# Performance work log

Measured on AMD Instinct MI355X. Metric: run time of the kernel, lower is better.

Reference implementation:

```python
import jax, jax.numpy as jnp
import numpy as np

B, S, HID, NH, HD = 2, 2048, 1024, 16, 64
SCALE = 1.0 / np.sqrt(HD)
NEG = -1e9


def _rope_cache(seq_len, dim, base=10000.0):
    inv_freq = 1.0 / (base ** (np.arange(0, dim, 2, dtype=np.float32) / dim))
    t = np.arange(seq_len, dtype=np.float32)
    freqs = np.outer(t, inv_freq)                      # [S, dim/2]
    emb = np.concatenate([freqs, freqs], axis=-1)      # [S, dim]
    return jnp.asarray(np.cos(emb)), jnp.asarray(np.sin(emb))


def _rotate_half(x):
    x1, x2 = jnp.split(x, 2, axis=-1)
    return jnp.concatenate([-x2, x1], axis=-1)


def setup_inputs() -> dict:
    key = jax.random.key(0)
    k0, k1, k2, k3, k4 = jax.random.split(key, 5)
    hidden_states = jax.random.normal(k0, (B, S, HID), jnp.float32)
    Wq = jax.random.normal(k1, (HID, NH * HD), jnp.float32) * 0.02
    Wk = jax.random.normal(k2, (HID, NH * HD), jnp.float32) * 0.02
    Wv = jax.random.normal(k3, (HID, NH * HD), jnp.float32) * 0.02
    Wo = jax.random.normal(k4, (NH * HD, HID), jnp.float32) * 0.02
    causal = jnp.tril(jnp.ones((S, S), bool))
    attention_mask = jnp.broadcast_to(
        jnp.where(causal, 0.0, NEG).astype(jnp.float32)[None, None], (B, 1, S, S))
    position_ids = jnp.broadcast_to(jnp.arange(S, dtype=jnp.int32)[None], (B, S))
    cos, sin = _rope_cache(S, HD)
    return {"hidden_states": hidden_states, "attention_mask": attention_mask,
            "position_ids": position_ids, "cos": cos, "sin": sin,
            "Wq": Wq, "Wk": Wk, "Wv": Wv, "Wo": Wo}


def reference(hidden_states, attention_mask, position_ids, cos, sin, Wq, Wk, Wv, Wo):
    b, s, _ = hidden_states.shape
    def proj(W):  # [B,S,HID] @ [HID,NH*HD] -> [B,NH,S,HD]
        return jnp.einsum('bsh,hd->bsd', hidden_states, W).reshape(b, s, NH, HD).transpose(0, 2, 1, 3)
    q, k, v = proj(Wq), proj(Wk), proj(Wv)
    # RoPE: gather per-position cos/sin -> [B,1,S,HD]
    cos_g = cos[position_ids][:, None]
    sin_g = sin[position_ids][:, None]
    q = q * cos_g + _rotate_half(q) * sin_g
    k = k * cos_g + _rotate_half(k) * sin_g
    scores = jnp.einsum('bhqd,bhkd->bhqk', q, k) * SCALE + attention_mask
    attn = jax.nn.softmax(scores.astype(jnp.float32), axis=-1).astype(q.dtype)
    out = jnp.einsum('bhqk,bhkd->bhqd', attn, v)
    out = out.transpose(0, 2, 1, 3).reshape(b, s, NH * HD)
    return jnp.einsum('bsd,dh->bsh', out, Wo)
```

## Files before the change

kernel.cpp:

```cpp
#include <hip/hip_runtime.h>

typedef __bf16 bf16x8 __attribute__((ext_vector_type(8)));
typedef float  f32x4  __attribute__((ext_vector_type(4)));
typedef unsigned short ushortx8 __attribute__((ext_vector_type(8)));
typedef unsigned short ushortx4 __attribute__((ext_vector_type(4)));

static __device__ __forceinline__ unsigned short f2bf(float f) {
  unsigned int u = __builtin_bit_cast(unsigned int, f);
  u += 0x7FFFu + ((u >> 16) & 1u);
  return (unsigned short)(u >> 16);
}
static __device__ __forceinline__ unsigned short f2bf_fast(float f) {
  unsigned int u = __builtin_bit_cast(unsigned int, f);
  return (unsigned short)((u + 0x8000u) >> 16);
}

#define GLL16(gp, lp) __builtin_amdgcn_global_load_lds(                       \
    (const __attribute__((address_space(1))) void*)(gp),                      \
    (__attribute__((address_space(3))) void*)(lp), 16, 0, 0)

__global__ __launch_bounds__(256) void cast_x_kernel(const float* __restrict__ x,
                                                     unsigned short* __restrict__ o) {
  long i = ((long)blockIdx.x * 256 + threadIdx.x) * 8;
  float4 f0 = *(const float4*)(x + i);
  float4 f1 = *(const float4*)(x + i + 4);
  ushortx8 u;
  u[0] = f2bf(f0.x); u[1] = f2bf(f0.y); u[2] = f2bf(f0.z); u[3] = f2bf(f0.w);
  u[4] = f2bf(f1.x); u[5] = f2bf(f1.y); u[6] = f2bf(f1.z); u[7] = f2bf(f1.w);
  *(ushortx8*)(o + i) = u;
}

__global__ __launch_bounds__(256) void tpose_w_kernel(const float* __restrict__ W0,
                                                      const float* __restrict__ W1,
                                                      const float* __restrict__ W2,
                                                      const float* __restrict__ W3,
                                                      unsigned short* __restrict__ D0,
                                                      unsigned short* __restrict__ D1,
                                                      unsigned short* __restrict__ D2,
                                                      unsigned short* __restrict__ D3) {
  int z = blockIdx.z;
  const float* src = (z == 0) ? W0 : (z == 1) ? W1 : (z == 2) ? W2 : W3;
  unsigned short* dst = (z == 0) ? D0 : (z == 1) ? D1 : (z == 2) ? D2 : D3;
  const int R = 1024, C = 1024;
  __shared__ unsigned short t[32][33];
  int c = blockIdx.x * 32 + threadIdx.x;
#pragma unroll
  for (int i = 0; i < 4; ++i) {
    int r = blockIdx.y * 32 + threadIdx.y + i * 8;
    t[threadIdx.y + i * 8][threadIdx.x] = f2bf(src[(size_t)r * C + c]);
  }
  __syncthreads();
  int rr = blockIdx.y * 32 + threadIdx.x;
#pragma unroll
  for (int i = 0; i < 4; ++i) {
    int cc = blockIdx.x * 32 + threadIdx.y + i * 8;
    dst[(size_t)cc * R + rr] = t[threadIdx.x][threadIdx.y + i * 8];
  }
}

__global__ __launch_bounds__(256) void tpose_kernel(const unsigned short* __restrict__ src,
                                                    unsigned short* __restrict__ dst,
                                                    int R, int C) {
  size_t moff = (size_t)blockIdx.z * (size_t)R * (size_t)C;
  src += moff; dst += moff;
  __shared__ unsigned short t[32][33];
  int c = blockIdx.x * 32 + threadIdx.x;
#pragma unroll
  for (int i = 0; i < 4; ++i) {
    int r = blockIdx.y * 32 + threadIdx.y + i * 8;
    t[threadIdx.y + i * 8][threadIdx.x] = src[(size_t)r * C + c];
  }
  __syncthreads();
  int rr = blockIdx.y * 32 + threadIdx.x;
#pragma unroll
  for (int i = 0; i < 4; ++i) {
    int cc = blockIdx.x * 32 + threadIdx.y + i * 8;
    dst[(size_t)cc * R + rr] = t[threadIdx.x][threadIdx.y + i * 8];
  }
}

template <int MODE>
__global__ __launch_bounds__(256) void gemm128_kernel(
    const unsigned short* __restrict__ A,
    const unsigned short* __restrict__ BT0,
    const unsigned short* __restrict__ BT1,
    const unsigned short* __restrict__ BT2,
    float* __restrict__ outF,
    unsigned short* __restrict__ outQ,
    unsigned short* __restrict__ outK,
    unsigned short* __restrict__ outV,
    const int* __restrict__ pos_ids,
    const float* __restrict__ cosb,
    const float* __restrict__ sinb) {
  const int K = 1024, N = 1024;
  int z = blockIdx.z;
  const unsigned short* BT = (MODE == 0 || z == 0) ? BT0 : (z == 1 ? BT1 : BT2);
  int n0 = blockIdx.x * 128, m0 = blockIdx.y * 128;
  int t = threadIdx.x, lane = t & 63, w = t >> 6;
  int wy = w >> 1, wx = w & 1;
  int n16 = lane & 15, quad = lane >> 4;
  __shared__ __align__(16) unsigned short sA[128 * 64];
  __shared__ __align__(16) unsigned short sB[128 * 64];

  int r8 = lane >> 3, c8 = lane & 7;
  int srow = w * 32 + r8;
  const char* gA = (const char*)(A + (size_t)(m0 + srow) * K) + (c8 ^ r8) * 16;
  const char* gB = (const char*)(BT + (size_t)(n0 + srow) * K) + (c8 ^ r8) * 16;

  f32x4 acc[4][4];
#pragma unroll
  for (int i = 0; i < 4; ++i)
#pragma unroll
    for (int j = 0; j < 4; ++j) acc[i][j] = f32x4{0.f, 0.f, 0.f, 0.f};

  for (int kk = 0; kk < K; kk += 64) {
    __syncthreads();
#pragma unroll
    for (int i = 0; i < 4; ++i) {
      GLL16(gA + (size_t)kk * 2 + (size_t)i * 8 * K * 2, sA + (w * 32 + i * 8) * 64);
      GLL16(gB + (size_t)kk * 2 + (size_t)i * 8 * K * 2, sB + (w * 32 + i * 8) * 64);
    }
    __syncthreads();
#pragma unroll
    for (int kb = 0; kb < 2; ++kb) {
      bf16x8 a[4], b[4];
#pragma unroll
      for (int i = 0; i < 4; ++i) {
        int ra = wy * 64 + i * 16 + n16;
        int rb = wx * 64 + i * 16 + n16;
        int cs = ((kb * 4 + quad) ^ (n16 & 7)) * 8;
        a[i] = *(const bf16x8*)(&sA[ra * 64 + cs]);
        b[i] = *(const bf16x8*)(&sB[rb * 64 + cs]);
      }
#pragma unroll
      for (int mt = 0; mt < 4; ++mt)
#pragma unroll
        for (int nt = 0; nt < 4; ++nt)
          acc[mt][nt] = __builtin_amdgcn_mfma_f32_16x16x32_bf16(a[mt], b[nt], acc[mt][nt], 0, 0, 0);
    }
  }

  if (MODE == 1 && z < 2) {
#pragma unroll
    for (int mt = 0; mt < 4; ++mt)
#pragma unroll
      for (int r = 0; r < 4; ++r) {
        int row = m0 + wy * 64 + mt * 16 + quad * 4 + r;
        int b = row >> 11, s = row & 2047;
        int pos = pos_ids[b * 2048 + s];
        const float* cb = cosb + (size_t)pos * 64;
        const float* sb = sinb + (size_t)pos * 64;
#pragma unroll
        for (int nt = 0; nt < 2; ++nt) {
          int d0 = nt * 16 + n16;
          float c0 = cb[d0], s0 = sb[d0], c1 = cb[d0 + 32], s1 = sb[d0 + 32];
          float x0 = acc[mt][nt][r], x1 = acc[mt][nt + 2][r];
          acc[mt][nt][r]     = x0 * c0 - x1 * s0;
          acc[mt][nt + 2][r] = x1 * c1 + x0 * s1;
        }
      }
  }

#pragma unroll
  for (int mt = 0; mt < 4; ++mt)
#pragma unroll
    for (int nt = 0; nt < 4; ++nt)
#pragma unroll
      for (int r = 0; r < 4; ++r) {
        int row = m0 + wy * 64 + mt * 16 + quad * 4 + r;
        int col = n0 + wx * 64 + nt * 16 + n16;
        float v = acc[mt][nt][r];
        if (MODE == 0) {
          outF[(size_t)row * N + col] = v;
        } else {
          unsigned short* dst = (z == 0) ? outQ : (z == 1 ? outK : outV);
          int b = row >> 11, s = row & 2047, h = col >> 6, d = col & 63;
          dst[(((size_t)b * 16 + h) * 2048 + s) * 64 + d] = f2bf(v);
        }
      }
}

__global__ __launch_bounds__(256) void attn_kernel(const unsigned short* __restrict__ Q,
                                                   const unsigned short* __restrict__ Kk,
                                                   const unsigned short* __restrict__ VT,
                                                   unsigned short* __restrict__ O) {
  int bh = blockIdx.x;
  int qt = (int)(gridDim.y - 1 - blockIdx.y);
  int t = threadIdx.x;
  int lane = t & 63;
  int w = t >> 6;
  int n16 = lane & 15, quad = lane >> 4;
  int r8 = lane >> 3, c8 = lane & 7;
  const unsigned short* Qb = Q + (size_t)bh * 2048 * 64;
  const unsigned short* Kb = Kk + (size_t)bh * 2048 * 64;
  const unsigned short* Vb = VT + (size_t)bh * 64 * 2048;

  __shared__ __align__(16) unsigned short sK0[64 * 64];
  __shared__ __align__(16) unsigned short sK1[64 * 64];
  __shared__ __align__(16) unsigned short sV0[64 * 64];
  __shared__ __align__(16) unsigned short sV1[64 * 64];
  __shared__ __align__(16) unsigned short sP[4][16 * 64];
  unsigned short* spW = sP[w];

  const float SCL2 = 0.125f * 1.44269504088896340736f;
  int b_ = bh >> 4, h_ = bh & 15;
  int nk = qt + 1;
  int qg = qt * 64 + w * 16 + n16;

  bf16x8 aQ[2];
#pragma unroll
  for (int kb = 0; kb < 2; ++kb)
    aQ[kb] = *(const bf16x8*)(Qb + (size_t)qg * 64 + kb * 32 + quad * 8);

  f32x4 o[4];
  float mst = -3e38f, lst = 0.f;
#pragma unroll
  for (int ct = 0; ct < 4; ++ct) o[ct] = f32x4{0.f, 0.f, 0.f, 0.f};

#define STAGE(kt_, SKB, SVB)                                                              \
  do {                                                                                    \
    const unsigned short* kg_ = Kb + (size_t)((kt_) * 64 + w * 16) * 64;                  \
    const unsigned short* vg_ = Vb + (size_t)(w * 16) * 2048 + (kt_) * 64;                \
    GLL16(kg_ + (size_t)r8 * 64 + (c8 ^ r8) * 8, &SKB[(w * 16) * 64]);                    \
    GLL16(kg_ + (size_t)(8 + r8) * 64 + (c8 ^ r8) * 8, &SKB[(w * 16 + 8) * 64]);          \
    GLL16(vg_ + (size_t)r8 * 2048 + (c8 ^ r8) * 8, &SVB[(w * 16) * 64]);                  \
    GLL16(vg_ + (size_t)(8 + r8) * 2048 + (c8 ^ r8) * 8, &SVB[(w * 16 + 8) * 64]);        \
  } while (0)

#define COMPUTE(kt_, SKB, SVB)                                                            \
  do {                                                                                    \
    f32x4 sc[4];                          \
    _Pragma("unroll") for (int mt = 0; mt < 4; ++mt) {                                    \
      const unsigned short* kr = &SKB[(mt * 16 + n16) * 64];                              \
      bf16x8 ka0 = *(const bf16x8*)(kr + ((quad ^ (n16 & 7)) * 8));                       \
      bf16x8 ka1 = *(const bf16x8*)(kr + (((4 + quad) ^ (n16 & 7)) * 8));                 \
      f32x4 zv = f32x4{0.f, 0.f, 0.f, 0.f};                                               \
      zv = __builtin_amdgcn_mfma_f32_16x16x32_bf16(ka0, aQ[0], zv, 0, 0, 0);              \
      sc[mt] = __builtin_amdgcn_mfma_f32_16x16x32_bf16(ka1, aQ[1], zv, 0, 0, 0);          \
    }                                                                                     \
    float p[4][4];                                                                        \
    _Pragma("unroll") for (int mt = 0; mt < 4; ++mt)                                      \
      _Pragma("unroll") for (int r = 0; r < 4; ++r) p[mt][r] = sc[mt][r] * SCL2;          \
    if ((kt_) == nk - 1) {                                 \
      int kb0 = (kt_) * 64 + quad * 4;                                                    \
      _Pragma("unroll") for (int mt = 0; mt < 4; ++mt)                                    \
        _Pragma("unroll") for (int r = 0; r < 4; ++r)                                     \
          if (kb0 + mt * 16 + r > qg) p[mt][r] = -3e38f;                                  \
    }                                                                                     \
    float rm = p[0][0];                                                                   \
    _Pragma("unroll") for (int mt = 0; mt < 4; ++mt)                                      \
      _Pragma("unroll") for (int r = 0; r < 4; ++r) rm = fmaxf(rm, p[mt][r]);             \
    rm = fmaxf(rm, __shfl_xor(rm, 16));                                                   \
    rm = fmaxf(rm, __shfl_xor(rm, 32));                                                   \
    float mn = fmaxf(mst, rm);                                                            \
    float al = exp2f(mst - mn);                                                           \
    mst = mn;                                                                             \
    float rs = 0.f;                                                                       \
    _Pragma("unroll") for (int mt = 0; mt < 4; ++mt)                                      \
      _Pragma("unroll") for (int r = 0; r < 4; ++r) {                                     \
        p[mt][r] = exp2f(p[mt][r] - mn);                                                  \
        rs += p[mt][r];                                                                   \
      }                                                                                   \
    lst = lst * al + rs;        \
    _Pragma("unroll") for (int ct = 0; ct < 4; ++ct)                                      \
      _Pragma("unroll") for (int r = 0; r < 4; ++r) o[ct][r] *= al;                       \
                   \
    _Pragma("unroll") for (int mt = 0; mt < 4; ++mt) {                                    \
      ushortx4 u;                                                                         \
      _Pragma("unroll") for (int r = 0; r < 4; ++r) u[r] = f2bf_fast(p[mt][r]);           \
      int ch = (mt * 2 + (quad >> 1)) ^ (n16 & 7);                                        \
      *(ushortx4*)(&spW[n16 * 64 + ch * 8 + (quad & 1) * 4]) = u;                         \
    }                                                                                     \
    __builtin_amdgcn_s_waitcnt(0xC07F);   \
    bf16x8 aP0 = *(const bf16x8*)(&spW[n16 * 64 + ((quad ^ (n16 & 7)) * 8)]);             \
    bf16x8 aP1 = *(const bf16x8*)(&spW[n16 * 64 + (((4 + quad) ^ (n16 & 7)) * 8)]);       \
    _Pragma("unroll") for (int ct = 0; ct < 4; ++ct) {                                    \
      const unsigned short* vr = &SVB[(ct * 16 + n16) * 64];                              \
      bf16x8 va0 = *(const bf16x8*)(vr + ((quad ^ (n16 & 7)) * 8));                       \
      bf16x8 va1 = *(const bf16x8*)(vr + (((4 + quad) ^ (n16 & 7)) * 8));                 \
      o[ct] = __builtin_amdgcn_mfma_f32_16x16x32_bf16(va0, aP0, o[ct], 0, 0, 0);          \
      o[ct] = __builtin_amdgcn_mfma_f32_16x16x32_bf16(va1, aP1, o[ct], 0, 0, 0);          \
    }                                                                                     \
  } while (0)

  STAGE(0, sK0, sV0);
  int kt = 0;
  while (true) {
    __syncthreads();
    if (kt + 1 < nk) STAGE(kt + 1, sK1, sV1);
    COMPUTE(kt, sK0, sV0);
    if (++kt == nk) break;
    __syncthreads();
    if (kt + 1 < nk) STAGE(kt + 1, sK0, sV0);
    COMPUTE(kt, sK1, sV1);
    if (++kt == nk) break;
  }
#undef STAGE
#undef COMPUTE

  lst += __shfl_xor(lst, 16);
  lst += __shfl_xor(lst, 32);
  float inv = 1.0f / lst;

#pragma unroll
  for (int ct = 0; ct < 4; ++ct) {
    ushortx4 u;
#pragma unroll
    for (int r = 0; r < 4; ++r) u[r] = f2bf(o[ct][r] * inv);
    size_t addr = ((size_t)b_ * 2048 + qg) * 1024 + h_ * 64 + ct * 16 + quad * 4;
    *(ushortx4*)(&O[addr]) = u;
  }
}

extern "C" void kernel_launch(void* const* d_in, const int* in_sizes, int n_in,
                              void* d_out, int out_size, void* d_ws, size_t ws_size,
                              hipStream_t stream) {
  const float* X    = (const float*)d_in[0];
  const int*   pos  = (const int*)d_in[2];
  const float* cosb = (const float*)d_in[3];
  const float* sinb = (const float*)d_in[4];
  const float* Wq   = (const float*)d_in[5];
  const float* Wk   = (const float*)d_in[6];
  const float* Wv   = (const float*)d_in[7];
  const float* Wo   = (const float*)d_in[8];
  float* out = (float*)d_out;

  char* ws = (char*)d_ws;
  const size_t SZ_X = 4096UL * 1024 * 2;
  const size_t SZ_W = 1024UL * 1024 * 2;
  unsigned short* Xbf = (unsigned short*)(ws);
  unsigned short* WTq = (unsigned short*)(ws + SZ_X);
  unsigned short* WTk = (unsigned short*)(ws + SZ_X + SZ_W);
  unsigned short* WTv = (unsigned short*)(ws + SZ_X + 2 * SZ_W);
  unsigned short* WTo = (unsigned short*)(ws + SZ_X + 3 * SZ_W);
  unsigned short* Qbf = (unsigned short*)(ws + SZ_X + 4 * SZ_W);
  unsigned short* Kbf = (unsigned short*)(ws + 2 * SZ_X + 4 * SZ_W);
  unsigned short* Vbf = (unsigned short*)(ws + 3 * SZ_X + 4 * SZ_W);
  unsigned short* VTr = (unsigned short*)(ws + 4 * SZ_X + 4 * SZ_W);
  unsigned short* Obf = (unsigned short*)(ws + 5 * SZ_X + 4 * SZ_W);

  cast_x_kernel<<<2048, 256, 0, stream>>>(X, Xbf);
  tpose_w_kernel<<<dim3(32, 32, 4), dim3(32, 8), 0, stream>>>(Wq, Wk, Wv, Wo,
                                                              WTq, WTk, WTv, WTo);

  gemm128_kernel<1><<<dim3(8, 32, 3), 256, 0, stream>>>(Xbf, WTq, WTk, WTv,
                                                        nullptr, Qbf, Kbf, Vbf,
                                                        pos, cosb, sinb);

  tpose_kernel<<<dim3(2, 64, 32), dim3(32, 8), 0, stream>>>(Vbf, VTr, 2048, 64);

  attn_kernel<<<dim3(32, 32), 256, 0, stream>>>(Qbf, Kbf, VTr, Obf);

  gemm128_kernel<0><<<dim3(8, 32, 1), 256, 0, stream>>>(Obf, WTo, nullptr, nullptr,
                                                        out, nullptr, nullptr, nullptr,
                                                        nullptr, nullptr, nullptr);
}
```

Before: 234.4 us.

## Split attention KV range across two wave groups, double-buffer GEMM, fuse prep kernels

The attention kernel now runs 512 threads per block. Two groups of four waves each process half of the causal key tiles for the same query tile, and their partial softmax states are merged through shared memory at the end. This is meant to raise parallelism and shorten the critical path of long causal rows. The GEMM main loop gets double-buffered LDS staging so global loads for the next k-tile overlap with MFMA compute. The X cast and weight transpose kernels are merged into a single launch. The cost is more LDS and higher register pressure per block, plus extra merge work and barriers.

```diff
diff --git a/kernel.cpp b/kernel.cpp
--- a/kernel.cpp
+++ b/kernel.cpp
@@ -19,26 +19,29 @@
     (const __attribute__((address_space(1))) void*)(gp),                      \
     (__attribute__((address_space(3))) void*)(lp), 16, 0, 0)
 
-__global__ __launch_bounds__(256) void cast_x_kernel(const float* __restrict__ x,
-                                                     unsigned short* __restrict__ o) {
-  long i = ((long)blockIdx.x * 256 + threadIdx.x) * 8;
-  float4 f0 = *(const float4*)(x + i);
-  float4 f1 = *(const float4*)(x + i + 4);
-  ushortx8 u;
-  u[0] = f2bf(f0.x); u[1] = f2bf(f0.y); u[2] = f2bf(f0.z); u[3] = f2bf(f0.w);
-  u[4] = f2bf(f1.x); u[5] = f2bf(f1.y); u[6] = f2bf(f1.z); u[7] = f2bf(f1.w);
-  *(ushortx8*)(o + i) = u;
-}
-
-__global__ __launch_bounds__(256) void tpose_w_kernel(const float* __restrict__ W0,
-                                                      const float* __restrict__ W1,
-                                                      const float* __restrict__ W2,
-                                                      const float* __restrict__ W3,
-                                                      unsigned short* __restrict__ D0,
-                                                      unsigned short* __restrict__ D1,
-                                                      unsigned short* __restrict__ D2,
-                                                      unsigned short* __restrict__ D3) {
+__global__ __launch_bounds__(256) void prep_kernel(const float* __restrict__ X,
+                                                   const float* __restrict__ W0,
+                                                   const float* __restrict__ W1,
+                                                   const float* __restrict__ W2,
+                                                   const float* __restrict__ W3,
+                                                   unsigned short* __restrict__ Xbf,
+                                                   unsigned short* __restrict__ D0,
+                                                   unsigned short* __restrict__ D1,
+                                                   unsigned short* __restrict__ D2,
+                                                   unsigned short* __restrict__ D3) {
   int z = blockIdx.z;
+  if (z >= 4) {
+    long bid = (long)(z - 4) * 1024 + blockIdx.y * 32 + blockIdx.x;
+    int tl = threadIdx.y * 32 + threadIdx.x;
+    long i = bid * 2048 + (long)tl * 8;
+    float4 f0 = *(const float4*)(X + i);
+    float4 f1 = *(const float4*)(X + i + 4);
+    ushortx8 u;
+    u[0] = f2bf(f0.x); u[1] = f2bf(f0.y); u[2] = f2bf(f0.z); u[3] = f2bf(f0.w);
+    u[4] = f2bf(f1.x); u[5] = f2bf(f1.y); u[6] = f2bf(f1.z); u[7] = f2bf(f1.w);
+    *(ushortx8*)(Xbf + i) = u;
+    return;
+  }
   const float* src = (z == 0) ? W0 : (z == 1) ? W1 : (z == 2) ? W2 : W3;
   unsigned short* dst = (z == 0) ? D0 : (z == 1) ? D1 : (z == 2) ? D2 : D3;
   const int R = 1024, C = 1024;
@@ -99,8 +102,10 @@
   int t = threadIdx.x, lane = t & 63, w = t >> 6;
   int wy = w >> 1, wx = w & 1;
   int n16 = lane & 15, quad = lane >> 4;
-  __shared__ __align__(16) unsigned short sA[128 * 64];
-  __shared__ __align__(16) unsigned short sB[128 * 64];
+  __shared__ __align__(16) unsigned short sA0[128 * 64];
+  __shared__ __align__(16) unsigned short sA1[128 * 64];
+  __shared__ __align__(16) unsigned short sB0[128 * 64];
+  __shared__ __align__(16) unsigned short sB1[128 * 64];
 
   int r8 = lane >> 3, c8 = lane & 7;
   int srow = w * 32 + r8;
@@ -113,32 +118,49 @@
 #pragma unroll
     for (int j = 0; j < 4; ++j) acc[i][j] = f32x4{0.f, 0.f, 0.f, 0.f};
 
-  for (int kk = 0; kk < K; kk += 64) {
+#define GSTAGE(kk_, SA, SB)                                                     \
+  do {                                                                          \
+    _Pragma("unroll") for (int i = 0; i < 4; ++i) {                             \
+      GLL16(gA + (size_t)(kk_) * 2 + (size_t)i * 8 * K * 2,                     \
+            SA + (w * 32 + i * 8) * 64);                                        \
+      GLL16(gB + (size_t)(kk_) * 2 + (size_t)i * 8 * K * 2,                     \
+            SB + (w * 32 + i * 8) * 64);                                        \
+    }                                                                           \
+  } while (0)
+
+#define GCOMPUTE(SA, SB)                                                        \
+  do {                                                                          \
+    _Pragma("unroll") for (int kb = 0; kb < 2; ++kb) {                          \
+      bf16x8 a[4], b[4];                                                        \
+      _Pragma("unroll") for (int i = 0; i < 4; ++i) {                           \
+        int ra = wy * 64 + i * 16 + n16;                                        \
+        int rb = wx * 64 + i * 16 + n16;                                        \
+        int cs = ((kb * 4 + quad) ^ (n16 & 7)) * 8;                             \
+        a[i] = *(const bf16x8*)(&SA[ra * 64 + cs]);                             \
+        b[i] = *(const bf16x8*)(&SB[rb * 64 + cs]);                             \
+      }                                                                         \
+      _Pragma("unroll") for (int mt = 0; mt < 4; ++mt)                          \
+        _Pragma("unroll") for (int nt = 0; nt < 4; ++nt)                        \
+          acc[mt][nt] =                                                         \
+              __builtin_amdgcn_mfma_f32_16x16x32_bf16(a[mt], b[nt],             \
+                                                      acc[mt][nt], 0, 0, 0);    \
+    }                                                                           \
+  } while (0)
+
+  GSTAGE(0, sA0, sB0);
+  for (int kk = 0; kk < K;) {
     __syncthreads();
-#pragma unroll
-    for (int i = 0; i < 4; ++i) {
-      GLL16(gA + (size_t)kk * 2 + (size_t)i * 8 * K * 2, sA + (w * 32 + i * 8) * 64);
-      GLL16(gB + (size_t)kk * 2 + (size_t)i * 8 * K * 2, sB + (w * 32 + i * 8) * 64);
-    }
+    if (kk + 64 < K) GSTAGE(kk + 64, sA1, sB1);
+    GCOMPUTE(sA0, sB0);
+    kk += 64;
+    if (kk >= K) break;
     __syncthreads();
-#pragma unroll
-    for (int kb = 0; kb < 2; ++kb) {
-      bf16x8 a[4], b[4];
-#pragma unroll
-      for (int i = 0; i < 4; ++i) {
-        int ra = wy * 64 + i * 16 + n16;
-        int rb = wx * 64 + i * 16 + n16;
-        int cs = ((kb * 4 + quad) ^ (n16 & 7)) * 8;
-        a[i] = *(const bf16x8*)(&sA[ra * 64 + cs]);
-        b[i] = *(const bf16x8*)(&sB[rb * 64 + cs]);
-      }
-#pragma unroll
-      for (int mt = 0; mt < 4; ++mt)
-#pragma unroll
-        for (int nt = 0; nt < 4; ++nt)
-          acc[mt][nt] = __builtin_amdgcn_mfma_f32_16x16x32_bf16(a[mt], b[nt], acc[mt][nt], 0, 0, 0);
-    }
-  }
+    if (kk + 64 < K) GSTAGE(kk + 64, sA0, sB0);
+    GCOMPUTE(sA1, sB1);
+    kk += 64;
+  }
+#undef GSTAGE
+#undef GCOMPUTE
 
   if (MODE == 1 && z < 2) {
 #pragma unroll
@@ -180,7 +202,7 @@
       }
 }
 
-__global__ __launch_bounds__(256) void attn_kernel(const unsigned short* __restrict__ Q,
+__global__ __launch_bounds__(512) void attn_kernel(const unsigned short* __restrict__ Q,
                                                    const unsigned short* __restrict__ Kk,
                                                    const unsigned short* __restrict__ VT,
                                                    unsigned short* __restrict__ O) {
@@ -189,23 +211,26 @@
   int t = threadIdx.x;
   int lane = t & 63;
   int w = t >> 6;
+  int g = w >> 2;
+  int w4 = w & 3;
   int n16 = lane & 15, quad = lane >> 4;
   int r8 = lane >> 3, c8 = lane & 7;
   const unsigned short* Qb = Q + (size_t)bh * 2048 * 64;
   const unsigned short* Kb = Kk + (size_t)bh * 2048 * 64;
   const unsigned short* Vb = VT + (size_t)bh * 64 * 2048;
 
-  __shared__ __align__(16) unsigned short sK0[64 * 64];
-  __shared__ __align__(16) unsigned short sK1[64 * 64];
-  __shared__ __align__(16) unsigned short sV0[64 * 64];
-  __shared__ __align__(16) unsigned short sV1[64 * 64];
-  __shared__ __align__(16) unsigned short sP[4][16 * 64];
+  __shared__ __align__(16) unsigned short sKV[2 * 2 * 2 * 4096];
+  __shared__ __align__(16) unsigned short sP[8][16 * 64];
   unsigned short* spW = sP[w];
+  unsigned short* gBase = sKV + g * 16384;
 
   const float SCL2 = 0.125f * 1.44269504088896340736f;
   int b_ = bh >> 4, h_ = bh & 15;
   int nk = qt + 1;
-  int qg = qt * 64 + w * 16 + n16;
+  int u = (nk + 1) >> 1;
+  int beg = g ? u : 0;
+  int end = g ? nk : u;
+  int qg = qt * 64 + w4 * 16 + n16;
 
   bf16x8 aQ[2];
 #pragma unroll
@@ -217,21 +242,27 @@
 #pragma unroll
   for (int ct = 0; ct < 4; ++ct) o[ct] = f32x4{0.f, 0.f, 0.f, 0.f};
 
-#define STAGE(kt_, SKB, SVB)                                                              \
+#define ASTAGE(kt_, BUF)                                                                  \
   do {                                                                                    \
-    const unsigned short* kg_ = Kb + (size_t)((kt_) * 64 + w * 16) * 64;                  \
-    const unsigned short* vg_ = Vb + (size_t)(w * 16) * 2048 + (kt_) * 64;                \
-    GLL16(kg_ + (size_t)r8 * 64 + (c8 ^ r8) * 8, &SKB[(w * 16) * 64]);                    \
-    GLL16(kg_ + (size_t)(8 + r8) * 64 + (c8 ^ r8) * 8, &SKB[(w * 16 + 8) * 64]);          \
-    GLL16(vg_ + (size_t)r8 * 2048 + (c8 ^ r8) * 8, &SVB[(w * 16) * 64]);                  \
-    GLL16(vg_ + (size_t)(8 + r8) * 2048 + (c8 ^ r8) * 8, &SVB[(w * 16 + 8) * 64]);        \
+    const unsigned short* kg_ = Kb + (size_t)((kt_) * 64 + w4 * 16) * 64;                 \
+    const unsigned short* vg_ = Vb + (size_t)(w4 * 16) * 2048 + (kt_) * 64;               \
+    unsigned short* dK = gBase + (BUF) * 8192 + (w4 * 16) * 64;                           \
+    unsigned short* dV = dK + 4096;                                                       \
+    GLL16(kg_ + (size_t)r8 * 64 + (c8 ^ r8) * 8, dK);                                     \
+    GLL16(kg_ + (size_t)(8 + r8) * 64 + (c8 ^ r8) * 8, dK + 8 * 64);                      \
+    GLL16(vg_ + (size_t)r8 * 2048 + (c8 ^ r8) * 8, dV);                                   \
+    GLL16(vg_ + (size_t)(8 + r8) * 2048 + (c8 ^ r8) * 8, dV + 8 * 64);                    \
   } while (0)
 
-#define COMPUTE(kt_, SKB, SVB)                                                            \
+#define ACOMPUTE(kt_, BUF)                                                                \
   do {                                                                                    \
-    f32x4 sc[4];                          \
+    const unsigned short* kB_ = gBase + (BUF) * 8192 + (w4 * 16) * 64 - (w4 * 16) * 64;   \
+    const unsigned short* kT_ = gBase + (BUF) * 8192;                                     \
+    const unsigned short* vT_ = kT_ + 4096;                                               \
+    (void)kB_;                                                                            \
+    f32x4 sc[4];                                \
     _Pragma("unroll") for (int mt = 0; mt < 4; ++mt) {                                    \
-      const unsigned short* kr = &SKB[(mt * 16 + n16) * 64];                              \
+      const unsigned short* kr = &kT_[(mt * 16 + n16) * 64];                              \
       bf16x8 ka0 = *(const bf16x8*)(kr + ((quad ^ (n16 & 7)) * 8));                       \
       bf16x8 ka1 = *(const bf16x8*)(kr + (((4 + quad) ^ (n16 & 7)) * 8));                 \
       f32x4 zv = f32x4{0.f, 0.f, 0.f, 0.f};                                               \
@@ -261,21 +292,20 @@
         p[mt][r] = exp2f(p[mt][r] - mn);                                                  \
         rs += p[mt][r];                                                                   \
       }                                                                                   \
-    lst = lst * al + rs;        \
+    lst = lst * al + rs;                                                                  \
     _Pragma("unroll") for (int ct = 0; ct < 4; ++ct)                                      \
       _Pragma("unroll") for (int r = 0; r < 4; ++r) o[ct][r] *= al;                       \
-                   \
     _Pragma("unroll") for (int mt = 0; mt < 4; ++mt) {                                    \
-      ushortx4 u;                                                                         \
-      _Pragma("unroll") for (int r = 0; r < 4; ++r) u[r] = f2bf_fast(p[mt][r]);           \
+      ushortx4 uu;                                                                        \
+      _Pragma("unroll") for (int r = 0; r < 4; ++r) uu[r] = f2bf_fast(p[mt][r]);          \
       int ch = (mt * 2 + (quad >> 1)) ^ (n16 & 7);                                        \
-      *(ushortx4*)(&spW[n16 * 64 + ch * 8 + (quad & 1) * 4]) = u;                         \
+      *(ushortx4*)(&spW[n16 * 64 + ch * 8 + (quad & 1) * 4]) = uu;                        \
     }                                                                                     \
-    __builtin_amdgcn_s_waitcnt(0xC07F);   \
+    __builtin_amdgcn_s_waitcnt(0xC07F);     \
     bf16x8 aP0 = *(const bf16x8*)(&spW[n16 * 64 + ((quad ^ (n16 & 7)) * 8)]);             \
     bf16x8 aP1 = *(const bf16x8*)(&spW[n16 * 64 + (((4 + quad) ^ (n16 & 7)) * 8)]);       \
     _Pragma("unroll") for (int ct = 0; ct < 4; ++ct) {                                    \
-      const unsigned short* vr = &SVB[(ct * 16 + n16) * 64];                              \
+      const unsigned short* vr = &vT_[(ct * 16 + n16) * 64];                              \
       bf16x8 va0 = *(const bf16x8*)(vr + ((quad ^ (n16 & 7)) * 8));                       \
       bf16x8 va1 = *(const bf16x8*)(vr + (((4 + quad) ^ (n16 & 7)) * 8));                 \
       o[ct] = __builtin_amdgcn_mfma_f32_16x16x32_bf16(va0, aP0, o[ct], 0, 0, 0);          \
@@ -283,32 +313,58 @@
     }                                                                                     \
   } while (0)
 
-  STAGE(0, sK0, sV0);
-  int kt = 0;
-  while (true) {
+  if (beg < end) ASTAGE(beg, 0);
+  int it = 0;
+  while (it < u) {
     __syncthreads();
-    if (kt + 1 < nk) STAGE(kt + 1, sK1, sV1);
-    COMPUTE(kt, sK0, sV0);
-    if (++kt == nk) break;
+    {
+      int kt = beg + it;
+      if (kt + 1 < end) ASTAGE(kt + 1, 1);
+      if (kt < end) ACOMPUTE(kt, 0);
+    }
+    if (++it >= u) break;
     __syncthreads();
-    if (kt + 1 < nk) STAGE(kt + 1, sK0, sV0);
-    COMPUTE(kt, sK1, sV1);
-    if (++kt == nk) break;
-  }
-#undef STAGE
-#undef COMPUTE
+    {
+      int kt = beg + it;
+      if (kt + 1 < end) ASTAGE(kt + 1, 0);
+      if (kt < end) ACOMPUTE(kt, 1);
+    }
+    ++it;
+  }
+#undef ASTAGE
+#undef ACOMPUTE
 
   lst += __shfl_xor(lst, 16);
   lst += __shfl_xor(lst, 32);
-  float inv = 1.0f / lst;
-
-#pragma unroll
-  for (int ct = 0; ct < 4; ++ct) {
-    ushortx4 u;
-#pragma unroll
-    for (int r = 0; r < 4; ++r) u[r] = f2bf(o[ct][r] * inv);
-    size_t addr = ((size_t)b_ * 2048 + qg) * 1024 + h_ * 64 + ct * 16 + quad * 4;
-    *(ushortx4*)(&O[addr]) = u;
+
+  __syncthreads();
+  float* scratch = (float*)sKV;
+  int sidx = (w4 * 64 + lane) * 18;
+  if (g == 1) {
+#pragma unroll
+    for (int ct = 0; ct < 4; ++ct)
+#pragma unroll
+      for (int r = 0; r < 4; ++r) scratch[sidx + ct * 4 + r] = o[ct][r];
+    scratch[sidx + 16] = mst;
+    scratch[sidx + 17] = lst;
+  }
+  __syncthreads();
+  if (g == 0) {
+    float m1 = scratch[sidx + 16], l1 = scratch[sidx + 17];
+    float m = fmaxf(mst, m1);
+    float a0 = exp2f(mst - m), a1 = exp2f(m1 - m);
+    float inv = 1.0f / (lst * a0 + l1 * a1);
+#pragma unroll
+    for (int ct = 0; ct < 4; ++ct) {
+      ushortx4 uo;
+#pragma unroll
+      for (int r = 0; r < 4; ++r) {
+        float v = (o[ct][r] * a0 + scratch[sidx + ct * 4 + r] * a1) * inv;
+        uo[r] = f2bf(v);
+      }
+      size_t addr = ((size_t)b_ * 2048 + qg) * 1024 + h_ * 64 + ct * 16 + quad * 4;
+      *(ushortx4*)(&O[addr]) = uo;
+    }
   }
 }
 
@@ -339,9 +395,8 @@
   unsigned short* VTr = (unsigned short*)(ws + 4 * SZ_X + 4 * SZ_W);
   unsigned short* Obf = (unsigned short*)(ws + 5 * SZ_X + 4 * SZ_W);
 
-  cast_x_kernel<<<2048, 256, 0, stream>>>(X, Xbf);
-  tpose_w_kernel<<<dim3(32, 32, 4), dim3(32, 8), 0, stream>>>(Wq, Wk, Wv, Wo,
-                                                              WTq, WTk, WTv, WTo);
+  prep_kernel<<<dim3(32, 32, 6), dim3(32, 8), 0, stream>>>(
+      X, Wq, Wk, Wv, Wo, Xbf, WTq, WTk, WTv, WTo);
 
   gemm128_kernel<1><<<dim3(8, 32, 3), 256, 0, stream>>>(Xbf, WTq, WTk, WTv,
                                                         nullptr, Qbf, Kbf, Vbf,
@@ -349,7 +404,7 @@
 
   tpose_kernel<<<dim3(2, 64, 32), dim3(32, 8), 0, stream>>>(Vbf, VTr, 2048, 64);
 
-  attn_kernel<<<dim3(32, 32), 256, 0, stream>>>(Qbf, Kbf, VTr, Obf);
+  attn_kernel<<<dim3(32, 32), 512, 0, stream>>>(Qbf, Kbf, VTr, Obf);
 
   gemm128_kernel<0><<<dim3(8, 32, 1), 256, 0, stream>>>(Obf, WTo, nullptr, nullptr,
                                                         out, nullptr, nullptr, nullptr,
```

Result: no change. 230.0 us (-1.9%).
